# Kernel optimization log

Hardware: AMD Instinct MI355X
Metric: run time of the kernel (lower is better)

## Reference

```python
import jax, jax.numpy as jnp
import numpy as np

H = 16  # n_heads

def setup_inputs() -> dict:
    key = jax.random.key(0)
    ks = jax.random.split(key, 8)
    B, S, D = 2, 2048, 1024
    q = jax.random.normal(ks[0], (B, S, D), dtype=jnp.float32)
    k = jax.random.normal(ks[1], (B, S, D), dtype=jnp.float32)
    v = jax.random.normal(ks[2], (B, S, D), dtype=jnp.float32)
    mask = jnp.ones((B, S, S), dtype=jnp.int32)
    scale = 1.0 / np.sqrt(D)
    Wq = jax.random.normal(ks[3], (D, D), dtype=jnp.float32) * scale
    Wk = jax.random.normal(ks[4], (D, D), dtype=jnp.float32) * scale
    Wv = jax.random.normal(ks[5], (D, D), dtype=jnp.float32) * scale
    Wo = jax.random.normal(ks[6], (D, D), dtype=jnp.float32) * scale
    return {"q": q, "k": k, "v": v, "mask": mask,
            "Wq": Wq, "Wk": Wk, "Wv": Wv, "Wo": Wo}

def reference(q, k, v, mask, Wq, Wk, Wv, Wo):
    B, S, D = q.shape
    dk = D // H
    # nn.Linear(bias=False): y = x @ W.T
    query = (q @ Wq.T).reshape(B, S, H, dk).transpose(0, 2, 1, 3)  # [B,H,S,dk]
    key_  = (k @ Wk.T).reshape(B, S, H, dk).transpose(0, 2, 1, 3)
    value = (v @ Wv.T).reshape(B, S, H, dk).transpose(0, 2, 1, 3)
    scores = jnp.einsum('bhqd,bhkd->bhqk', query, key_) / jnp.sqrt(jnp.float32(dk))
    scores = jnp.where(mask[:, None, :, :] == 0, jnp.float32(-1e9), scores)
    attn = jax.nn.softmax(scores, axis=-1)  # dropout=0.0 -> identity
    x = jnp.einsum('bhqk,bhkd->bhqd', attn, value)  # [B,H,S,dk]
    x = x.transpose(0, 2, 1, 3).reshape(B, S, D)
    return x @ Wo.T
```

## Files before the change

kernel.cpp:

```cpp
#include <hip/hip_runtime.h>
#include <hip/hip_bf16.h>

#define B_ 2
#define S_ 2048
#define D_ 1024
#define H_ 16

typedef __bf16 bf16x8 __attribute__((ext_vector_type(8)));
typedef __bf16 bf16x4v __attribute__((ext_vector_type(4)));
typedef float f32x4 __attribute__((ext_vector_type(4)));
typedef float f32x16 __attribute__((ext_vector_type(16)));

__device__ __forceinline__ float exp2fast(float x) {
  return __builtin_amdgcn_exp2f(x);
}

__device__ __forceinline__ float max3f(float a, float b, float c) {
  return fmaxf(fmaxf(a, b), c);
}

__device__ __forceinline__ unsigned short f2bf(float f) {
  unsigned int u = __float_as_uint(f);
  u += 0x7fff + ((u >> 16) & 1);
  return (unsigned short)(u >> 16);
}

__device__ __forceinline__ unsigned int pk2(float x, float y) {
  unsigned int r;
  asm("v_cvt_pk_bf16_f32 %0, %1, %2" : "=v"(r) : "v"(x), "v"(y));
  return r;
}

__device__ __forceinline__ void gload_lds16(const void* g, void* l) {
  __builtin_amdgcn_global_load_lds(
      (const __attribute__((address_space(1))) void*)g,
      (__attribute__((address_space(3))) void*)l, 16, 0, 0);
}

__global__ __launch_bounds__(256) void prep(
    const float* __restrict__ q, const float* __restrict__ k,
    const float* __restrict__ v, const int* __restrict__ mask,
    const float* __restrict__ Wq, const float* __restrict__ Wk,
    const float* __restrict__ Wv, const float* __restrict__ Wo,
    unsigned short* __restrict__ qb, unsigned short* __restrict__ kb,
    unsigned short* __restrict__ vb,
    unsigned short* __restrict__ Wqb, unsigned short* __restrict__ Wkb,
    unsigned short* __restrict__ Wvb, unsigned short* __restrict__ Wob,
    int* __restrict__ flag) {
  const int z = blockIdx.z;
  const int stride = gridDim.x * blockDim.x;
  const int tid0 = blockIdx.x * blockDim.x + threadIdx.x;
  if (z < 3) {
    const float* s = z == 0 ? q : (z == 1 ? k : v);
    unsigned short* d = z == 0 ? qb : (z == 1 ? kb : vb);
    const int n4 = B_ * S_ * D_ / 4;
    for (int i = tid0; i < n4; i += stride) {
      float4 f = ((const float4*)s)[i];
      ushort4 o;
      o.x = f2bf(f.x); o.y = f2bf(f.y); o.z = f2bf(f.z); o.w = f2bf(f.w);
      ((ushort4*)d)[i] = o;
    }
  } else if (z == 3) {
    const int n4 = D_ * D_ / 4;
#pragma unroll
    for (int t = 0; t < 4; t++) {
      const float* s = t == 0 ? Wq : (t == 1 ? Wk : (t == 2 ? Wv : Wo));
      unsigned short* d = t == 0 ? Wqb : (t == 1 ? Wkb : (t == 2 ? Wvb : Wob));
      for (int i = tid0; i < n4; i += stride) {
        float4 f = ((const float4*)s)[i];
        ushort4 o;
        o.x = f2bf(f.x); o.y = f2bf(f.y); o.z = f2bf(f.z); o.w = f2bf(f.w);
        ((ushort4*)d)[i] = o;
      }
    }
  } else {
    const int half = B_ * S_ * S_ / 8;
    const int base = (z - 4) * half;
    bool zf = false;
    for (int i = tid0; i < half; i += stride) {
      int4 mv = ((const int4*)mask)[base + i];
      zf |= (mv.x == 0) || (mv.y == 0) || (mv.z == 0) || (mv.w == 0);
    }
    if (__any(zf)) {
      if ((threadIdx.x & 63) == 0) atomicOr(flag, 1);
    }
  }
}

__device__ __forceinline__ void gemm_core(
    const unsigned short* __restrict__ A, const unsigned short* __restrict__ W,
    unsigned short* As, unsigned short* Bs, int rowBase, int colBase,
    f32x4 (&acc)[4][4]) {
  const int tid = threadIdx.x, lane = tid & 63, w = tid >> 6;
  const int wm = w >> 1, wn = w & 1, l15 = lane & 15, l4 = lane >> 4;
  for (int kt = 0; kt < 16; ++kt) {
#pragma unroll
    for (int i = 0; i < 4; i++) {
      int chunk = (w * 4 + i) * 64 + lane;
      int row = chunk >> 3, c = chunk & 7;
      int cs = c ^ (row & 7);
      gload_lds16(A + (size_t)(rowBase + row) * 1024 + kt * 64 + cs * 8,
                  (char*)As + (w * 4 + i) * 1024);
      gload_lds16(W + (size_t)(colBase + row) * 1024 + kt * 64 + cs * 8,
                  (char*)Bs + (w * 4 + i) * 1024);
    }
    __syncthreads();
#pragma unroll
    for (int ks = 0; ks < 2; ks++) {
      bf16x8 af[4], bfr[4];
#pragma unroll
      for (int mi = 0; mi < 4; mi++) {
        int row = wm * 64 + mi * 16 + l15;
        af[mi] = *(const bf16x8*)((const char*)As + row * 128 +
                                  (((ks * 4 + l4) ^ (row & 7)) << 4));
      }
#pragma unroll
      for (int ni = 0; ni < 4; ni++) {
        int row = wn * 64 + ni * 16 + l15;
        bfr[ni] = *(const bf16x8*)((const char*)Bs + row * 128 +
                                   (((ks * 4 + l4) ^ (row & 7)) << 4));
      }
#pragma unroll
      for (int mi = 0; mi < 4; mi++)
#pragma unroll
        for (int ni = 0; ni < 4; ni++)
          acc[mi][ni] = __builtin_amdgcn_mfma_f32_16x16x32_bf16(
              af[mi], bfr[ni], acc[mi][ni], 0, 0, 0);
    }
    __syncthreads();
  }
}

__global__ __launch_bounds__(256, 2) void gemm_qkv(
    const unsigned short* __restrict__ qA, const unsigned short* __restrict__ kA,
    const unsigned short* __restrict__ vA,
    const unsigned short* __restrict__ Wq, const unsigned short* __restrict__ Wk,
    const unsigned short* __restrict__ Wv,
    unsigned short* __restrict__ Qp, unsigned short* __restrict__ Kp,
    unsigned short* __restrict__ Vtp) {
  __shared__ unsigned short As[128 * 64], Bs[128 * 64];
  const int z = blockIdx.z;
  const unsigned short* A = z == 0 ? qA : (z == 1 ? kA : vA);
  const unsigned short* W = z == 0 ? Wq : (z == 1 ? Wk : Wv);
  const int rowBase = blockIdx.y * 128, colBase = blockIdx.x * 128;
  f32x4 acc[4][4] = {};
  gemm_core(A, W, As, Bs, rowBase, colBase, acc);
  const int tid = threadIdx.x, lane = tid & 63, w = tid >> 6;
  const int wm = w >> 1, wn = w & 1, l15 = lane & 15, l4 = lane >> 4;
#pragma unroll
  for (int mi = 0; mi < 4; mi++)
#pragma unroll
    for (int ni = 0; ni < 4; ni++)
#pragma unroll
      for (int r = 0; r < 4; r++) {
        int gr = rowBase + wm * 64 + mi * 16 + l4 * 4 + r;
        int gc = colBase + wn * 64 + ni * 16 + l15;
        int b = gr >> 11, s = gr & 2047, h = gc >> 6, d = gc & 63;
        float v = acc[mi][ni][r];
        if (z == 0)
          Qp[(((size_t)(b * 16 + h) * 2048 + s) << 6) + d] =
              f2bf(v * 0.18033688011112042f);
        else if (z == 1)
          Kp[(((size_t)(b * 16 + h) * 2048 + s) << 6) + d] = f2bf(v);
        else
          Vtp[((size_t)(b * 16 + h) * 64 + d) * 2048 + s] = f2bf(v);
      }
}

__global__ __launch_bounds__(256, 2) void gemm_o(
    const unsigned short* __restrict__ A, const unsigned short* __restrict__ W,
    float* __restrict__ Out) {
  __shared__ unsigned short As[128 * 64], Bs[64 * 64];
  const int rowBase = blockIdx.y * 128, colBase = blockIdx.x * 64;
  const int tid = threadIdx.x, lane = tid & 63, w = tid >> 6;
  const int wm = w >> 1, wn = w & 1, l15 = lane & 15, l4 = lane >> 4;
  f32x4 acc[4][2] = {};
  for (int kt = 0; kt < 16; ++kt) {
#pragma unroll
    for (int i = 0; i < 4; i++) {
      int chunk = (w * 4 + i) * 64 + lane;
      int row = chunk >> 3, c = chunk & 7;
      int cs = c ^ (row & 7);
      gload_lds16(A + (size_t)(rowBase + row) * 1024 + kt * 64 + cs * 8,
                  (char*)As + (w * 4 + i) * 1024);
    }
#pragma unroll
    for (int i = 0; i < 2; i++) {
      int chunk = (w * 2 + i) * 64 + lane;
      int row = chunk >> 3, c = chunk & 7;
      int cs = c ^ (row & 7);
      gload_lds16(W + (size_t)(colBase + row) * 1024 + kt * 64 + cs * 8,
                  (char*)Bs + (w * 2 + i) * 1024);
    }
    __syncthreads();
#pragma unroll
    for (int ks = 0; ks < 2; ks++) {
      bf16x8 af[4], bfr[2];
#pragma unroll
      for (int mi = 0; mi < 4; mi++) {
        int row = wm * 64 + mi * 16 + l15;
        af[mi] = *(const bf16x8*)((const char*)As + row * 128 +
                                  (((ks * 4 + l4) ^ (row & 7)) << 4));
      }
#pragma unroll
      for (int ni = 0; ni < 2; ni++) {
        int row = wn * 32 + ni * 16 + l15;
        bfr[ni] = *(const bf16x8*)((const char*)Bs + row * 128 +
                                   (((ks * 4 + l4) ^ (row & 7)) << 4));
      }
#pragma unroll
      for (int mi = 0; mi < 4; mi++)
#pragma unroll
        for (int ni = 0; ni < 2; ni++)
          acc[mi][ni] = __builtin_amdgcn_mfma_f32_16x16x32_bf16(
              af[mi], bfr[ni], acc[mi][ni], 0, 0, 0);
    }
    __syncthreads();
  }
#pragma unroll
  for (int mi = 0; mi < 4; mi++)
#pragma unroll
    for (int ni = 0; ni < 2; ni++)
#pragma unroll
      for (int r = 0; r < 4; r++) {
        int gr = rowBase + wm * 64 + mi * 16 + l4 * 4 + r;
        int gc = colBase + wn * 32 + ni * 16 + l15;
        Out[(size_t)gr * 1024 + gc] = acc[mi][ni][r];
      }
}

__global__ __launch_bounds__(256, 2) void attn(
    const unsigned short* __restrict__ Qp, const unsigned short* __restrict__ Kp,
    const unsigned short* __restrict__ Vt, unsigned short* __restrict__ Xo,
    const int* __restrict__ flag, const int* __restrict__ mask) {
  __shared__ unsigned short Ks[2][64 * 64];
  __shared__ unsigned short Vs[2][64 * 64];
  const int tid = threadIdx.x, lane = tid & 63, w = tid >> 6;
  const int l31 = lane & 31, hi = lane >> 5;
  const int bid = ((blockIdx.x & 7) << 6) + (blockIdx.x >> 3);
  const int qblk = bid & 15;
  const int bh = bid >> 4;
  const int h = bh & 15, b = bh >> 4;
  const int q = qblk * 128 + w * 32 + l31;
  const int hz = *flag;

  const unsigned short* Kbase = Kp + (size_t)bh * S_ * 64;
  const unsigned short* Vbase = Vt + (size_t)bh * 64 * S_;

  bf16x8 qf[4];
#pragma unroll
  for (int ds = 0; ds < 4; ds++)
    qf[ds] = *(const bf16x8*)(Qp + ((size_t)bh * S_ + q) * 64 + ds * 16 + hi * 8);

  union { unsigned int u[4]; bf16x8 v; } ones;
  ones.u[0] = ones.u[1] = ones.u[2] = ones.u[3] = 0x3F803F80u;

  float m = -__builtin_inff();
  f32x16 lsum = {};
  f32x16 accO[2] = {};

  auto stage = [&](int kt, int buf) {
#pragma unroll
    for (int i = 0; i < 2; i++) {
      int ch = (w * 2 + i) * 64 + lane;
      int row = ch >> 3, c = ch & 7;
      int cs = c ^ (row & 7);
      gload_lds16(Kbase + (size_t)(kt * 64 + row) * 64 + cs * 8,
                  (char*)&Ks[buf][0] + (w * 2 + i) * 1024);
      gload_lds16(Vbase + (size_t)row * S_ + kt * 64 + cs * 8,
                  (char*)&Vs[buf][0] + (w * 2 + i) * 1024);
    }
  };

  auto body = [&](int kt, int cbuf) {
    f32x16 s[2] = {};
    __builtin_amdgcn_s_setprio(1);
#pragma unroll
    for (int ds = 0; ds < 4; ds++)
#pragma unroll
      for (int kb = 0; kb < 2; kb++) {
        int row = kb * 32 + l31;
        bf16x8 kf = *(const bf16x8*)((const char*)&Ks[cbuf][0] + row * 128 +
                                     (((ds * 2 + hi) ^ (row & 7)) << 4));
        s[kb] = __builtin_amdgcn_mfma_f32_32x32x16_bf16(kf, qf[ds], s[kb], 0, 0, 0);
      }
    __builtin_amdgcn_s_setprio(0);

    if (hz) {
#pragma unroll
      for (int kb = 0; kb < 2; kb++)
#pragma unroll
        for (int i = 0; i < 16; i++) {
          int kc = kt * 64 + kb * 32 + (i & 3) + 8 * (i >> 2) + 4 * hi;
          if (mask[((size_t)b * S_ + q) * S_ + kc] == 0) s[kb][i] = -1e9f;
        }
    }

    float a0 = max3f(s[0][0], s[0][1], s[0][2]);
    float a1 = max3f(s[0][3], s[0][4], s[0][5]);
    float a2 = max3f(s[0][6], s[0][7], s[0][8]);
    float a3 = max3f(s[0][9], s[0][10], s[0][11]);
    float a4 = max3f(s[0][12], s[0][13], s[0][14]);
    float a5 = max3f(s[0][15], s[1][0], s[1][1]);
    float a6 = max3f(s[1][2], s[1][3], s[1][4]);
    float a7 = max3f(s[1][5], s[1][6], s[1][7]);
    float a8 = max3f(s[1][8], s[1][9], s[1][10]);
    float a9 = max3f(s[1][11], s[1][12], s[1][13]);
    float aa = fmaxf(s[1][14], s[1][15]);
    float b0 = max3f(a0, a1, a2);
    float b1 = max3f(a3, a4, a5);
    float b2 = max3f(a6, a7, a8);
    float b3 = max3f(a9, aa, b0);
    float mx = max3f(b1, b2, b3);
    mx = fmaxf(mx, __shfl_xor(mx, 32));

    if (!__all(mx - m <= 8.f)) {
      float mn = fmaxf(m, mx);
      float al = exp2fast(m - mn);
      m = mn;
      lsum[0] *= al;
#pragma unroll
      for (int db = 0; db < 2; db++)
#pragma unroll
        for (int i = 0; i < 16; i++) accO[db][i] *= al;
    }

#pragma unroll
    for (int kb = 0; kb < 2; kb++)
#pragma unroll
      for (int i = 0; i < 16; i++) s[kb][i] = exp2fast(s[kb][i] - m);

#pragma unroll
    for (int ks2 = 0; ks2 < 4; ks2++) {
      union { unsigned int u[4]; bf16x8 v; } pb;
      {
        const int kb = ks2 >> 1;
        const int gb = (ks2 & 1) * 8;
        unsigned int a0u = pk2(s[kb][gb + 0], s[kb][gb + 1]);
        unsigned int a1u = pk2(s[kb][gb + 2], s[kb][gb + 3]);
        unsigned int b0u = pk2(s[kb][gb + 4], s[kb][gb + 5]);
        unsigned int b1u = pk2(s[kb][gb + 6], s[kb][gb + 7]);
        unsigned int t0 = hi ? a0u : b0u;
        unsigned int t1 = hi ? a1u : b1u;
        unsigned int r0 = __shfl_xor(t0, 32);
        unsigned int r1 = __shfl_xor(t1, 32);
        pb.u[0] = hi ? r0 : a0u;
        pb.u[1] = hi ? r1 : a1u;
        pb.u[2] = hi ? b0u : r0;
        pb.u[3] = hi ? b1u : r1;
      }
      __builtin_amdgcn_s_setprio(1);
      lsum = __builtin_amdgcn_mfma_f32_32x32x16_bf16(ones.v, pb.v, lsum, 0, 0, 0);
#pragma unroll
      for (int db = 0; db < 2; db++) {
        int row = db * 32 + l31;
        bf16x8 vf = *(const bf16x8*)((const char*)&Vs[cbuf][0] + row * 128 +
                                     (((ks2 * 2 + hi) ^ (row & 7)) << 4));
        accO[db] = __builtin_amdgcn_mfma_f32_32x32x16_bf16(vf, pb.v, accO[db], 0, 0, 0);
      }
      __builtin_amdgcn_s_setprio(0);
    }
  };

  stage(0, 0);
  for (int kt2 = 0; kt2 < 32; kt2 += 2) {
    __syncthreads();
    stage(kt2 + 1, 1);
    body(kt2, 0);
    __syncthreads();
    if (kt2 + 2 < 32) stage(kt2 + 2, 0);
    body(kt2 + 1, 1);
  }

  float rl = 1.0f / lsum[0];
  const size_t orow = (((size_t)(b * S_ + q)) << 10) + h * 64;
#pragma unroll
  for (int db = 0; db < 2; db++)
#pragma unroll
    for (int rq = 0; rq < 4; rq++) {
      bf16x4v o;
#pragma unroll
      for (int j = 0; j < 4; j++) o[j] = (__bf16)(accO[db][rq * 4 + j] * rl);
      *(bf16x4v*)(Xo + orow + db * 32 + rq * 8 + hi * 4) = o;
    }
}

extern "C" void kernel_launch(void* const* d_in, const int* in_sizes, int n_in,
                              void* d_out, int out_size, void* d_ws, size_t ws_size,
                              hipStream_t stream) {
  const float* q = (const float*)d_in[0];
  const float* k = (const float*)d_in[1];
  const float* v = (const float*)d_in[2];
  const int* mask = (const int*)d_in[3];
  const float* Wq = (const float*)d_in[4];
  const float* Wk = (const float*)d_in[5];
  const float* Wv = (const float*)d_in[6];
  const float* Wo = (const float*)d_in[7];

  char* ws = (char*)d_ws;
  const size_t MB = 1024 * 1024;
  unsigned short* qb16 = (unsigned short*)(ws);
  unsigned short* kb16 = (unsigned short*)(ws + 8 * MB);
  unsigned short* vb16 = (unsigned short*)(ws + 16 * MB);
  unsigned short* Wq16 = (unsigned short*)(ws + 24 * MB);
  unsigned short* Wk16 = (unsigned short*)(ws + 26 * MB);
  unsigned short* Wv16 = (unsigned short*)(ws + 28 * MB);
  unsigned short* Wo16 = (unsigned short*)(ws + 30 * MB);
  unsigned short* Qp = (unsigned short*)(ws + 32 * MB);
  unsigned short* Kp = (unsigned short*)(ws + 40 * MB);
  unsigned short* Vtp = (unsigned short*)(ws + 48 * MB);
  int* flag = (int*)(ws + 56 * MB);
  unsigned short* Xo = qb16;

  (void)hipMemsetAsync(flag, 0, 4, stream);
  prep<<<dim3(1024, 1, 6), 256, 0, stream>>>(q, k, v, mask, Wq, Wk, Wv, Wo,
                                             qb16, kb16, vb16, Wq16, Wk16, Wv16,
                                             Wo16, flag);
  gemm_qkv<<<dim3(8, 32, 3), 256, 0, stream>>>(qb16, kb16, vb16, Wq16, Wk16, Wv16,
                                               Qp, Kp, Vtp);
  attn<<<dim3(512), 256, 0, stream>>>(Qp, Kp, Vtp, Xo, flag, mask);
  gemm_o<<<dim3(16, 32), 256, 0, stream>>>(Xo, Wo16, (float*)d_out);
}
```

Before: 143.7 us.

## Rewrite QKV projection GEMM with 256x256 tiles and double-buffered ping-pong pipeline

Replaces the 128x128 QKV GEMM with an 8-wave, 256x256-tile kernel that double-buffers LDS and issues global-to-LDS loads for the next K tile while MFMAs run on the current one. Each iteration is split into four phases with barriers and setprio so that wave groups alternate between loading and compute. The goal is to hide global memory latency and raise per-block data reuse. In exchange, the grid drops to 192 blocks (fewer than the CU count) at one block per CU, and it uses 128KB of LDS per block.

Measured after the change: 161.1 us. 12.1% more time.

```diff
diff --git a/kernel.cpp b/kernel.cpp
--- a/kernel.cpp
+++ b/kernel.cpp
@@ -87,74 +87,151 @@
   }
 }
 
-__device__ __forceinline__ void gemm_core(
-    const unsigned short* __restrict__ A, const unsigned short* __restrict__ W,
-    unsigned short* As, unsigned short* Bs, int rowBase, int colBase,
-    f32x4 (&acc)[4][4]) {
-  const int tid = threadIdx.x, lane = tid & 63, w = tid >> 6;
-  const int wm = w >> 1, wn = w & 1, l15 = lane & 15, l4 = lane >> 4;
-  for (int kt = 0; kt < 16; ++kt) {
-#pragma unroll
-    for (int i = 0; i < 4; i++) {
-      int chunk = (w * 4 + i) * 64 + lane;
-      int row = chunk >> 3, c = chunk & 7;
-      int cs = c ^ (row & 7);
-      gload_lds16(A + (size_t)(rowBase + row) * 1024 + kt * 64 + cs * 8,
-                  (char*)As + (w * 4 + i) * 1024);
-      gload_lds16(W + (size_t)(colBase + row) * 1024 + kt * 64 + cs * 8,
-                  (char*)Bs + (w * 4 + i) * 1024);
-    }
-    __syncthreads();
-#pragma unroll
-    for (int ks = 0; ks < 2; ks++) {
-      bf16x8 af[4], bfr[4];
-#pragma unroll
-      for (int mi = 0; mi < 4; mi++) {
-        int row = wm * 64 + mi * 16 + l15;
-        af[mi] = *(const bf16x8*)((const char*)As + row * 128 +
-                                  (((ks * 4 + l4) ^ (row & 7)) << 4));
-      }
-#pragma unroll
-      for (int ni = 0; ni < 4; ni++) {
-        int row = wn * 64 + ni * 16 + l15;
-        bfr[ni] = *(const bf16x8*)((const char*)Bs + row * 128 +
-                                   (((ks * 4 + l4) ^ (row & 7)) << 4));
-      }
-#pragma unroll
-      for (int mi = 0; mi < 4; mi++)
-#pragma unroll
-        for (int ni = 0; ni < 4; ni++)
-          acc[mi][ni] = __builtin_amdgcn_mfma_f32_16x16x32_bf16(
-              af[mi], bfr[ni], acc[mi][ni], 0, 0, 0);
-    }
-    __syncthreads();
-  }
-}
-
-__global__ __launch_bounds__(256, 2) void gemm_qkv(
+__global__ __launch_bounds__(512, 1) void gemm_qkv8(
     const unsigned short* __restrict__ qA, const unsigned short* __restrict__ kA,
     const unsigned short* __restrict__ vA,
     const unsigned short* __restrict__ Wq, const unsigned short* __restrict__ Wk,
     const unsigned short* __restrict__ Wv,
     unsigned short* __restrict__ Qp, unsigned short* __restrict__ Kp,
     unsigned short* __restrict__ Vtp) {
-  __shared__ unsigned short As[128 * 64], Bs[128 * 64];
+  __shared__ unsigned short As[2][2][128 * 64];
+  __shared__ unsigned short Bs[2][2][128 * 64];
+  const int tid = threadIdx.x, lane = tid & 63, wid = tid >> 6;
+  const int wr = wid >> 2, wc = wid & 3;
+  const int l15 = lane & 15, l4 = lane >> 4;
   const int z = blockIdx.z;
   const unsigned short* A = z == 0 ? qA : (z == 1 ? kA : vA);
   const unsigned short* W = z == 0 ? Wq : (z == 1 ? Wk : Wv);
-  const int rowBase = blockIdx.y * 128, colBase = blockIdx.x * 128;
-  f32x4 acc[4][4] = {};
-  gemm_core(A, W, As, Bs, rowBase, colBase, acc);
-  const int tid = threadIdx.x, lane = tid & 63, w = tid >> 6;
-  const int wm = w >> 1, wn = w & 1, l15 = lane & 15, l4 = lane >> 4;
-#pragma unroll
-  for (int mi = 0; mi < 4; mi++)
+  const int rowBase = blockIdx.y * 256, colBase = blockIdx.x * 256;
+
+  f32x4 acc[8][4] = {};
+
+  auto stageJ = [&](int kt, int dbuf, int j) {
+    int c = ((j & 1) << 9) + tid;
+    int row = c >> 3;
+    int slot = (c & 7) ^ (row & 7);
+    int ht = j >> 1, half = ht & 1;
+    const unsigned short* src =
+        (ht < 2) ? A + (size_t)(rowBase + half * 128 + row) * 1024 + kt * 64 + slot * 8
+                 : W + (size_t)(colBase + half * 128 + row) * 1024 + kt * 64 + slot * 8;
+    unsigned short* dst = (ht < 2) ? &As[dbuf][half][0] : &Bs[dbuf][half][0];
+    gload_lds16(src, (char*)dst + (((j & 1) << 9) + (wid << 6)) * 16);
+  };
+  auto rdA = [&](int dbuf, int mi, int ks) -> bf16x8 {
+    int row = mi * 16 + l15;
+    int slot = (ks * 4 + l4) ^ (row & 7);
+    return *(const bf16x8*)((const char*)&As[dbuf][wr][0] + row * 128 + slot * 16);
+  };
+  auto rdB = [&](int dbuf, int ni, int ks) -> bf16x8 {
+    int row = (wc & 1) * 64 + ni * 16 + l15;
+    int slot = (ks * 4 + l4) ^ (row & 7);
+    return *(const bf16x8*)((const char*)&Bs[dbuf][wc >> 1][0] + row * 128 + slot * 16);
+  };
+
+#define FENCE_TOP()                                          \
+  do {                                                       \
+    asm volatile("s_waitcnt vmcnt(0)" ::: "memory");         \
+    __builtin_amdgcn_sched_barrier(0);                       \
+    __builtin_amdgcn_s_barrier();                            \
+    __builtin_amdgcn_sched_barrier(0);                       \
+  } while (0)
+#define PHASE_BAR()                                          \
+  do {                                                       \
+    __builtin_amdgcn_s_barrier();                            \
+    asm volatile("s_waitcnt lgkmcnt(0)" ::: "memory");       \
+    __builtin_amdgcn_sched_barrier(0);                       \
+  } while (0)
+#define PHASE_END()                                          \
+  do {                                                       \
+    __builtin_amdgcn_sched_barrier(0);                       \
+    __builtin_amdgcn_s_barrier();                            \
+  } while (0)
+
+  auto iter = [&](int kt, int dbuf, bool doStage) {
+    FENCE_TOP();
+    bf16x8 a03[4][2], a47[4][2], bb[4][2];
+#pragma unroll
+    for (int mi = 0; mi < 4; mi++) { a03[mi][0] = rdA(dbuf, mi, 0); a03[mi][1] = rdA(dbuf, mi, 1); }
+#pragma unroll
+    for (int ni = 0; ni < 2; ni++) { bb[ni][0] = rdB(dbuf, ni, 0); bb[ni][1] = rdB(dbuf, ni, 1); }
+    if (doStage) { stageJ(kt + 1, dbuf ^ 1, 0); stageJ(kt + 1, dbuf ^ 1, 1);
+                   stageJ(kt + 1, dbuf ^ 1, 2); stageJ(kt + 1, dbuf ^ 1, 3); }
+    PHASE_BAR();
+    __builtin_amdgcn_s_setprio(1);
+#pragma unroll
+    for (int mi = 0; mi < 4; mi++)
+#pragma unroll
+      for (int ni = 0; ni < 2; ni++)
+#pragma unroll
+        for (int ks = 0; ks < 2; ks++)
+          acc[mi][ni] = __builtin_amdgcn_mfma_f32_16x16x32_bf16(
+              a03[mi][ks], bb[ni][ks], acc[mi][ni], 0, 0, 0);
+    __builtin_amdgcn_s_setprio(0);
+    PHASE_END();
+#pragma unroll
+    for (int ni = 2; ni < 4; ni++) { bb[ni][0] = rdB(dbuf, ni, 0); bb[ni][1] = rdB(dbuf, ni, 1); }
+    if (doStage) { stageJ(kt + 1, dbuf ^ 1, 4); stageJ(kt + 1, dbuf ^ 1, 5);
+                   stageJ(kt + 1, dbuf ^ 1, 6); stageJ(kt + 1, dbuf ^ 1, 7); }
+    PHASE_BAR();
+    __builtin_amdgcn_s_setprio(1);
+#pragma unroll
+    for (int mi = 0; mi < 4; mi++)
+#pragma unroll
+      for (int ni = 2; ni < 4; ni++)
+#pragma unroll
+        for (int ks = 0; ks < 2; ks++)
+          acc[mi][ni] = __builtin_amdgcn_mfma_f32_16x16x32_bf16(
+              a03[mi][ks], bb[ni][ks], acc[mi][ni], 0, 0, 0);
+    __builtin_amdgcn_s_setprio(0);
+    PHASE_END();
+#pragma unroll
+    for (int mi = 0; mi < 4; mi++) { a47[mi][0] = rdA(dbuf, mi + 4, 0); a47[mi][1] = rdA(dbuf, mi + 4, 1); }
+    PHASE_BAR();
+    __builtin_amdgcn_s_setprio(1);
+#pragma unroll
+    for (int mi = 0; mi < 4; mi++)
+#pragma unroll
+      for (int ni = 2; ni < 4; ni++)
+#pragma unroll
+        for (int ks = 0; ks < 2; ks++)
+          acc[mi + 4][ni] = __builtin_amdgcn_mfma_f32_16x16x32_bf16(
+              a47[mi][ks], bb[ni][ks], acc[mi + 4][ni], 0, 0, 0);
+    __builtin_amdgcn_s_setprio(0);
+    PHASE_END();
+    PHASE_BAR();
+    __builtin_amdgcn_s_setprio(1);
+#pragma unroll
+    for (int mi = 0; mi < 4; mi++)
+#pragma unroll
+      for (int ni = 0; ni < 2; ni++)
+#pragma unroll
+        for (int ks = 0; ks < 2; ks++)
+          acc[mi + 4][ni] = __builtin_amdgcn_mfma_f32_16x16x32_bf16(
+              a47[mi][ks], bb[ni][ks], acc[mi + 4][ni], 0, 0, 0);
+    __builtin_amdgcn_s_setprio(0);
+    PHASE_END();
+  };
+
+#pragma unroll
+  for (int j = 0; j < 8; j++) stageJ(0, 0, j);
+  __syncthreads();
+
+  for (int kt2 = 0; kt2 < 16; kt2 += 2) {
+    iter(kt2, 0, kt2 < 15);
+    iter(kt2 + 1, 1, kt2 + 1 < 15);
+  }
+#undef FENCE_TOP
+#undef PHASE_BAR
+#undef PHASE_END
+
+#pragma unroll
+  for (int mi = 0; mi < 8; mi++)
 #pragma unroll
     for (int ni = 0; ni < 4; ni++)
 #pragma unroll
       for (int r = 0; r < 4; r++) {
-        int gr = rowBase + wm * 64 + mi * 16 + l4 * 4 + r;
-        int gc = colBase + wn * 64 + ni * 16 + l15;
+        int gr = rowBase + wr * 128 + mi * 16 + l4 * 4 + r;
+        int gc = colBase + wc * 64 + ni * 16 + l15;
         int b = gr >> 11, s = gr & 2047, h = gc >> 6, d = gc & 63;
         float v = acc[mi][ni][r];
         if (z == 0)
@@ -416,8 +493,8 @@
   prep<<<dim3(1024, 1, 6), 256, 0, stream>>>(q, k, v, mask, Wq, Wk, Wv, Wo,
                                              qb16, kb16, vb16, Wq16, Wk16, Wv16,
                                              Wo16, flag);
-  gemm_qkv<<<dim3(8, 32, 3), 256, 0, stream>>>(qb16, kb16, vb16, Wq16, Wk16, Wv16,
-                                               Qp, Kp, Vtp);
+  gemm_qkv8<<<dim3(4, 16, 3), 512, 0, stream>>>(qb16, kb16, vb16, Wq16, Wk16, Wv16,
+                                                Qp, Kp, Vtp);
   attn<<<dim3(512), 256, 0, stream>>>(Qp, Kp, Vtp, Xo, flag, mask);
   gemm_o<<<dim3(16, 32), 256, 0, stream>>>(Xo, Wo16, (float*)d_out);
 }
```

## Fuse fp32-to-bf16 activation conversion into QKV GEMM A-tile loads

Applied to the files above, without the earlier changes.

Removes the separate conversion pass that wrote bf16 copies of q, k and v. The QKV GEMM now reads fp32 activations directly, packs them to bf16 in registers and stores them into the swizzled LDS tile. This avoids writing and re-reading 24 MB of intermediate data, but the A-tile loads become synchronous register loads instead of direct global-to-LDS transfers, and each block re-converts its A rows once per column tile. The V-transpose store is also vectorized to 4-element bf16 writes.

After: 152.1 us. 5.8% more time.

```diff
diff --git a/kernel.cpp b/kernel.cpp
--- a/kernel.cpp
+++ b/kernel.cpp
@@ -38,29 +38,16 @@
 }
 
 __global__ __launch_bounds__(256) void prep(
-    const float* __restrict__ q, const float* __restrict__ k,
-    const float* __restrict__ v, const int* __restrict__ mask,
+    const int* __restrict__ mask,
     const float* __restrict__ Wq, const float* __restrict__ Wk,
     const float* __restrict__ Wv, const float* __restrict__ Wo,
-    unsigned short* __restrict__ qb, unsigned short* __restrict__ kb,
-    unsigned short* __restrict__ vb,
     unsigned short* __restrict__ Wqb, unsigned short* __restrict__ Wkb,
     unsigned short* __restrict__ Wvb, unsigned short* __restrict__ Wob,
     int* __restrict__ flag) {
   const int z = blockIdx.z;
   const int stride = gridDim.x * blockDim.x;
   const int tid0 = blockIdx.x * blockDim.x + threadIdx.x;
-  if (z < 3) {
-    const float* s = z == 0 ? q : (z == 1 ? k : v);
-    unsigned short* d = z == 0 ? qb : (z == 1 ? kb : vb);
-    const int n4 = B_ * S_ * D_ / 4;
-    for (int i = tid0; i < n4; i += stride) {
-      float4 f = ((const float4*)s)[i];
-      ushort4 o;
-      o.x = f2bf(f.x); o.y = f2bf(f.y); o.z = f2bf(f.z); o.w = f2bf(f.w);
-      ((ushort4*)d)[i] = o;
-    }
-  } else if (z == 3) {
+  if (z == 0) {
     const int n4 = D_ * D_ / 4;
 #pragma unroll
     for (int t = 0; t < 4; t++) {
@@ -75,7 +62,7 @@
     }
   } else {
     const int half = B_ * S_ * S_ / 8;
-    const int base = (z - 4) * half;
+    const int base = (z - 1) * half;
     bool zf = false;
     for (int i = tid0; i < half; i += stride) {
       int4 mv = ((const int4*)mask)[base + i];
@@ -87,84 +74,93 @@
   }
 }
 
-__device__ __forceinline__ void gemm_core(
-    const unsigned short* __restrict__ A, const unsigned short* __restrict__ W,
-    unsigned short* As, unsigned short* Bs, int rowBase, int colBase,
-    f32x4 (&acc)[4][4]) {
-  const int tid = threadIdx.x, lane = tid & 63, w = tid >> 6;
-  const int wm = w >> 1, wn = w & 1, l15 = lane & 15, l4 = lane >> 4;
-  for (int kt = 0; kt < 16; ++kt) {
-#pragma unroll
-    for (int i = 0; i < 4; i++) {
-      int chunk = (w * 4 + i) * 64 + lane;
-      int row = chunk >> 3, c = chunk & 7;
-      int cs = c ^ (row & 7);
-      gload_lds16(A + (size_t)(rowBase + row) * 1024 + kt * 64 + cs * 8,
-                  (char*)As + (w * 4 + i) * 1024);
-      gload_lds16(W + (size_t)(colBase + row) * 1024 + kt * 64 + cs * 8,
-                  (char*)Bs + (w * 4 + i) * 1024);
-    }
-    __syncthreads();
-#pragma unroll
-    for (int ks = 0; ks < 2; ks++) {
-      bf16x8 af[4], bfr[4];
-#pragma unroll
-      for (int mi = 0; mi < 4; mi++) {
-        int row = wm * 64 + mi * 16 + l15;
-        af[mi] = *(const bf16x8*)((const char*)As + row * 128 +
-                                  (((ks * 4 + l4) ^ (row & 7)) << 4));
-      }
-#pragma unroll
-      for (int ni = 0; ni < 4; ni++) {
-        int row = wn * 64 + ni * 16 + l15;
-        bfr[ni] = *(const bf16x8*)((const char*)Bs + row * 128 +
-                                   (((ks * 4 + l4) ^ (row & 7)) << 4));
-      }
-#pragma unroll
-      for (int mi = 0; mi < 4; mi++)
-#pragma unroll
-        for (int ni = 0; ni < 4; ni++)
-          acc[mi][ni] = __builtin_amdgcn_mfma_f32_16x16x32_bf16(
-              af[mi], bfr[ni], acc[mi][ni], 0, 0, 0);
-    }
-    __syncthreads();
-  }
-}
-
 __global__ __launch_bounds__(256, 2) void gemm_qkv(
-    const unsigned short* __restrict__ qA, const unsigned short* __restrict__ kA,
-    const unsigned short* __restrict__ vA,
+    const float* __restrict__ qA, const float* __restrict__ kA,
+    const float* __restrict__ vA,
     const unsigned short* __restrict__ Wq, const unsigned short* __restrict__ Wk,
     const unsigned short* __restrict__ Wv,
     unsigned short* __restrict__ Qp, unsigned short* __restrict__ Kp,
     unsigned short* __restrict__ Vtp) {
   __shared__ unsigned short As[128 * 64], Bs[128 * 64];
   const int z = blockIdx.z;
-  const unsigned short* A = z == 0 ? qA : (z == 1 ? kA : vA);
+  const float* A = z == 0 ? qA : (z == 1 ? kA : vA);
   const unsigned short* W = z == 0 ? Wq : (z == 1 ? Wk : Wv);
   const int rowBase = blockIdx.y * 128, colBase = blockIdx.x * 128;
-  f32x4 acc[4][4] = {};
-  gemm_core(A, W, As, Bs, rowBase, colBase, acc);
   const int tid = threadIdx.x, lane = tid & 63, w = tid >> 6;
   const int wm = w >> 1, wn = w & 1, l15 = lane & 15, l4 = lane >> 4;
+  f32x4 acc[4][4] = {};
+
+  for (int kt = 0; kt < 16; ++kt) {
+#pragma unroll
+    for (int i = 0; i < 4; i++) {
+      int chunk = (w * 4 + i) * 64 + lane;
+      int row = chunk >> 3, c = chunk & 7;
+      int cs = c ^ (row & 7);
+      gload_lds16(W + (size_t)(colBase + row) * 1024 + kt * 64 + cs * 8,
+                  (char*)Bs + (w * 4 + i) * 1024);
+    }
+#pragma unroll
+    for (int i = 0; i < 8; i++) {
+      int li = i * 256 + tid;
+      int row = li >> 4, c4 = li & 15;
+      float4 f = *(const float4*)(A + (size_t)(rowBase + row) * 1024 +
+                                  kt * 64 + c4 * 4);
+      uint2 p;
+      p.x = pk2(f.x, f.y);
+      p.y = pk2(f.z, f.w);
+      int slot = (c4 >> 1) ^ (row & 7);
+      *(uint2*)((char*)As + row * 128 + slot * 16 + (c4 & 1) * 8) = p;
+    }
+    __syncthreads();
+#pragma unroll
+    for (int ks = 0; ks < 2; ks++) {
+      bf16x8 af[4], bfr[4];
+#pragma unroll
+      for (int mi = 0; mi < 4; mi++) {
+        int row = wm * 64 + mi * 16 + l15;
+        af[mi] = *(const bf16x8*)((const char*)As + row * 128 +
+                                  (((ks * 4 + l4) ^ (row & 7)) << 4));
+      }
+#pragma unroll
+      for (int ni = 0; ni < 4; ni++) {
+        int row = wn * 64 + ni * 16 + l15;
+        bfr[ni] = *(const bf16x8*)((const char*)Bs + row * 128 +
+                                   (((ks * 4 + l4) ^ (row & 7)) << 4));
+      }
+#pragma unroll
+      for (int mi = 0; mi < 4; mi++)
+#pragma unroll
+        for (int ni = 0; ni < 4; ni++)
+          acc[mi][ni] = __builtin_amdgcn_mfma_f32_16x16x32_bf16(
+              af[mi], bfr[ni], acc[mi][ni], 0, 0, 0);
+    }
+    __syncthreads();
+  }
+
 #pragma unroll
   for (int mi = 0; mi < 4; mi++)
 #pragma unroll
-    for (int ni = 0; ni < 4; ni++)
-#pragma unroll
-      for (int r = 0; r < 4; r++) {
-        int gr = rowBase + wm * 64 + mi * 16 + l4 * 4 + r;
-        int gc = colBase + wn * 64 + ni * 16 + l15;
-        int b = gr >> 11, s = gr & 2047, h = gc >> 6, d = gc & 63;
-        float v = acc[mi][ni][r];
-        if (z == 0)
-          Qp[(((size_t)(b * 16 + h) * 2048 + s) << 6) + d] =
-              f2bf(v * 0.18033688011112042f);
-        else if (z == 1)
-          Kp[(((size_t)(b * 16 + h) * 2048 + s) << 6) + d] = f2bf(v);
-        else
-          Vtp[((size_t)(b * 16 + h) * 64 + d) * 2048 + s] = f2bf(v);
-      }
+    for (int ni = 0; ni < 4; ni++) {
+      int gr0 = rowBase + wm * 64 + mi * 16 + l4 * 4;
+      int gc = colBase + wn * 64 + ni * 16 + l15;
+      int b = gr0 >> 11, s0 = gr0 & 2047, h = gc >> 6, d = gc & 63;
+      if (z == 2) {
+        bf16x4v o;
+#pragma unroll
+        for (int r = 0; r < 4; r++) o[r] = (__bf16)acc[mi][ni][r];
+        *(bf16x4v*)(Vtp + ((size_t)(b * 16 + h) * 64 + d) * 2048 + s0) = o;
+      } else {
+#pragma unroll
+        for (int r = 0; r < 4; r++) {
+          float v = acc[mi][ni][r];
+          if (z == 0)
+            Qp[(((size_t)(b * 16 + h) * 2048 + s0 + r) << 6) + d] =
+                f2bf(v * 0.18033688011112042f);
+          else
+            Kp[(((size_t)(b * 16 + h) * 2048 + s0 + r) << 6) + d] = f2bf(v);
+        }
+      }
+    }
 }
 
 __global__ __launch_bounds__(256, 2) void gemm_o(
@@ -399,9 +395,7 @@
 
   char* ws = (char*)d_ws;
   const size_t MB = 1024 * 1024;
-  unsigned short* qb16 = (unsigned short*)(ws);
-  unsigned short* kb16 = (unsigned short*)(ws + 8 * MB);
-  unsigned short* vb16 = (unsigned short*)(ws + 16 * MB);
+  unsigned short* Xo = (unsigned short*)(ws);
   unsigned short* Wq16 = (unsigned short*)(ws + 24 * MB);
   unsigned short* Wk16 = (unsigned short*)(ws + 26 * MB);
   unsigned short* Wv16 = (unsigned short*)(ws + 28 * MB);
@@ -410,13 +404,11 @@
   unsigned short* Kp = (unsigned short*)(ws + 40 * MB);
   unsigned short* Vtp = (unsigned short*)(ws + 48 * MB);
   int* flag = (int*)(ws + 56 * MB);
-  unsigned short* Xo = qb16;
 
   (void)hipMemsetAsync(flag, 0, 4, stream);
-  prep<<<dim3(1024, 1, 6), 256, 0, stream>>>(q, k, v, mask, Wq, Wk, Wv, Wo,
-                                             qb16, kb16, vb16, Wq16, Wk16, Wv16,
-                                             Wo16, flag);
-  gemm_qkv<<<dim3(8, 32, 3), 256, 0, stream>>>(qb16, kb16, vb16, Wq16, Wk16, Wv16,
+  prep<<<dim3(1024, 1, 3), 256, 0, stream>>>(mask, Wq, Wk, Wv, Wo,
+                                             Wq16, Wk16, Wv16, Wo16, flag);
+  gemm_qkv<<<dim3(8, 32, 3), 256, 0, stream>>>(q, k, v, Wq16, Wk16, Wv16,
                                                Qp, Kp, Vtp);
   attn<<<dim3(512), 256, 0, stream>>>(Qp, Kp, Vtp, Xo, flag, mask);
   gemm_o<<<dim3(16, 32), 256, 0, stream>>>(Xo, Wo16, (float*)d_out);
```
